# Performance work log

Measured on AMD Instinct MI355X. Metric: run time of the kernel, lower is better.

The kernel has to match this reference:

```python
import jax, jax.numpy as jnp
import numpy as np

S, B, D, H, FF, L, V, O = 512, 32, 512, 8, 2048, 6, 32000, 1000
DH = D // H
EPS = 1e-5


def layer_norm(x, g, b):
    mu = jnp.mean(x, axis=-1, keepdims=True)
    var = jnp.mean((x - mu) ** 2, axis=-1, keepdims=True)
    return (x - mu) * jax.lax.rsqrt(var + EPS) * g + b


def positional_encoding(seq_len, dim):
    pos = np.arange(seq_len, dtype=np.float32)[:, None]
    i = np.arange(dim)
    angle = pos / (10000.0 ** ((i // 2 * 2.0) / dim))
    pe = np.where(i % 2 == 0, np.sin(angle), np.cos(angle)).astype(np.float32)
    return jnp.asarray(pe)  # [seq_len, dim]


def setup_inputs() -> dict:
    key = jax.random.key(0)
    ks = jax.random.split(key, 16)
    sc = 0.02
    inp = {
        'x': jax.random.randint(ks[0], (S, B), 0, V, dtype=jnp.int32),
        'x_len': jnp.full((B,), S, dtype=jnp.int32),
        'emb': jax.random.normal(ks[1], (V, D), jnp.float32) * sc,
        'Wq': jax.random.normal(ks[2], (L, D, D), jnp.float32) * sc,
        'bq': jnp.zeros((L, D), jnp.float32),
        'Wk': jax.random.normal(ks[3], (L, D, D), jnp.float32) * sc,
        'bk': jnp.zeros((L, D), jnp.float32),
        'Wv': jax.random.normal(ks[4], (L, D, D), jnp.float32) * sc,
        'bv': jnp.zeros((L, D), jnp.float32),
        'Wo': jax.random.normal(ks[5], (L, D, D), jnp.float32) * sc,
        'bo': jnp.zeros((L, D), jnp.float32),
        'ln1_g': jnp.ones((L, D), jnp.float32),
        'ln1_b': jnp.zeros((L, D), jnp.float32),
        'W1': jax.random.normal(ks[6], (L, D, FF), jnp.float32) * sc,
        'b1': jnp.zeros((L, FF), jnp.float32),
        'W2': jax.random.normal(ks[7], (L, FF, D), jnp.float32) * sc,
        'b2': jnp.zeros((L, D), jnp.float32),
        'ln2_g': jnp.ones((L, D), jnp.float32),
        'ln2_b': jnp.zeros((L, D), jnp.float32),
        'W_fc': jax.random.normal(ks[8], (S * D, O), jnp.float32) * sc,
        'b_fc': jnp.zeros((O,), jnp.float32),
    }
    return inp


def reference(x, x_len, emb, Wq, bq, Wk, bk, Wv, bv, Wo, bo, ln1_g, ln1_b,
              W1, b1, W2, b2, ln2_g, ln2_b, W_fc, b_fc):
    out = emb[x]                      # [S, B, D]
    out = jnp.transpose(out, (1, 0, 2))  # [B, S, D]
    out = out + positional_encoding(S, D)[None, :, :]
    scale = DH ** -0.5
    for l in range(L):
        # NOTE: faithful to the original buggy head-split: plain row-major
        # reshape [B,S,D] -> [B*H,S,DH] without a [B,H,S,DH] transpose.
        q = jnp.reshape(out @ Wq[l] + bq[l], (B * H, S, DH))
        k = jnp.reshape(out @ Wk[l] + bk[l], (B * H, S, DH))
        v = jnp.reshape(out @ Wv[l] + bv[l], (B * H, S, DH))
        attn = jax.nn.softmax(jnp.einsum('gqd,gkd->gqk', q, k) * scale, axis=-1)
        ctx = jnp.einsum('gqk,gkd->gqd', attn, v).reshape(B, S, D)
        h = layer_norm(ctx @ Wo[l] + bo[l] + out, ln1_g[l], ln1_b[l])
        f = jax.nn.relu(h @ W1[l] + b1[l]) @ W2[l] + b2[l]
        out = layer_norm(f + h, ln2_g[l], ln2_b[l])
    out = out.reshape(B, S * D)
    return out @ W_fc + b_fc          # [B, O]
```

## Files before the change

### kernel.cpp

```cpp
#include <hip/hip_runtime.h>
#include <cstdint>
#include <cstddef>

#define S_  512
#define B_  32
#define D_  512
#define FF_ 2048
#define L_  6
#define O_  1000
#define M_  (B_*S_)
#define G_  256
#define DH_ 64

typedef __attribute__((ext_vector_type(8))) short bf16x8;
typedef __attribute__((ext_vector_type(4))) float f32x4;
typedef __attribute__((ext_vector_type(16))) float f32x16;

__device__ __forceinline__ unsigned short f2bf(float f) {
  unsigned int u = __builtin_bit_cast(unsigned int, f);
  u = (u + 0x7fffu + ((u >> 16) & 1u)) >> 16;
  return (unsigned short)u;
}
__device__ __forceinline__ float bf2f(unsigned short u) {
  return __builtin_bit_cast(float, (unsigned int)u << 16);
}
__device__ __forceinline__ unsigned int pkbf(float a, float b) {
  return (unsigned int)f2bf(a) | ((unsigned int)f2bf(b) << 16);
}
__device__ __forceinline__ unsigned int prm(float a, float b) {
  return __builtin_amdgcn_perm(__builtin_bit_cast(unsigned int, b),
                               __builtin_bit_cast(unsigned int, a), 0x07060302u);
}
__device__ __forceinline__ void gload_lds16(const void* g, void* l) {
  __builtin_amdgcn_global_load_lds(
      (const __attribute__((address_space(1))) unsigned int*)g,
      (__attribute__((address_space(3))) unsigned int*)l, 16, 0, 0);
}

__global__ void pe_kernel(float* __restrict__ pe) {
  int i = blockIdx.x * 256 + threadIdx.x;
  int s = i >> 9, d = i & 511;
  double de = (double)(d & ~1);
  double ang = (double)s * exp(de * (-9.210340371976184 / 512.0));
  pe[i] = (d & 1) ? (float)cos(ang) : (float)sin(ang);
}

__global__ void wconv_kernel(const float* __restrict__ W, unsigned short* __restrict__ Wt,
                             int K, int N, size_t ozs) {
  __shared__ float tile[32][33];
  const float* Wl = W + (size_t)blockIdx.z * K * N;
  unsigned short* Wtl = Wt + (size_t)blockIdx.z * ozs;
  int k0 = blockIdx.x * 32, n0 = blockIdx.y * 32;
  int c = threadIdx.x & 31, rb = threadIdx.x >> 5;
#pragma unroll
  for (int i = 0; i < 4; ++i) {
    int r = rb + i * 8;
    tile[r][c] = Wl[(size_t)(k0 + r) * N + n0 + c];
  }
  __syncthreads();
#pragma unroll
  for (int i = 0; i < 4; ++i) {
    int r = rb + i * 8;
    Wtl[(size_t)(n0 + r) * K + k0 + c] = f2bf(tile[c][r]);
  }
}

__global__ void embed_kernel(const int* __restrict__ x, const float* __restrict__ emb,
                             const float* __restrict__ pe, unsigned short* __restrict__ xb) {
  int bi = blockIdx.x;
  int s = bi / B_, b = bi % B_;
  int tok = x[s * B_ + b];
  int d = threadIdx.x * 4;
  float4 e = *(const float4*)(emb + (size_t)tok * D_ + d);
  float4 p = *(const float4*)(pe + (size_t)s * D_ + d);
  size_t o = ((size_t)b * S_ + s) * D_ + d;
  ushort4 u;
  u.x = f2bf(e.x + p.x); u.y = f2bf(e.y + p.y);
  u.z = f2bf(e.z + p.z); u.w = f2bf(e.w + p.w);
  *(ushort4*)(xb + o) = u;
}

__global__ __launch_bounds__(256, 2) void gemm_kernel(
    const unsigned short* __restrict__ A, const unsigned short* __restrict__ Bt,
    const float* __restrict__ b0, const float* __restrict__ b1, const float* __restrict__ b2,
    unsigned short* __restrict__ o0, unsigned short* __restrict__ o1, unsigned short* __restrict__ o2,
    int K, int N, int relu, int split, int nbx) {
  __shared__ unsigned short As[3][128 * 32];
  __shared__ unsigned short Bs[3][256 * 32];
  int nwg = nbx * (M_ / 128);
  int cpx = nwg >> 3;
  int id = blockIdx.x;
  int wg = (id & 7) * cpx + (id >> 3);
  int bx = wg % nbx, by = wg / nbx;
  int m0 = by * 128, n0 = bx * 256;

  int tid = threadIdx.x, lane = tid & 63, wid = tid >> 6;
  f32x4 acc[8][4];
#pragma unroll
  for (int mi = 0; mi < 8; ++mi)
#pragma unroll
    for (int ni = 0; ni < 4; ++ni) acc[mi][ni] = (f32x4)0.0f;

  int srow = lane >> 2, scol = (lane & 3) * 8;
  const unsigned short* Abase = A + (size_t)m0 * K;
  const unsigned short* Bbase = Bt + (size_t)n0 * K;
  int c16 = lane & 15, hi = lane >> 4;
  int koff = hi * 8;
  int brow = wid * 64 + c16;
  int nk = K >> 5;

  auto STAGE = [&](int kt, int bb) {
    int k0 = kt * 32;
#pragma unroll
    for (int i = 0; i < 6; ++i) {
      int c = wid * 6 + i;
      if (c < 8) {
        gload_lds16(Abase + (size_t)(c * 16 + srow) * K + k0 + scol, (char*)As[bb] + c * 1024);
      } else {
        int c2 = c - 8;
        gload_lds16(Bbase + (size_t)(c2 * 16 + srow) * K + k0 + scol, (char*)Bs[bb] + c2 * 1024);
      }
    }
  };

  STAGE(0, 0); STAGE(1, 1); STAGE(2, 2);
  int bb = 0;
  for (int kt = 0; kt < nk; ++kt) {
    int rem = nk - 1 - kt;
    if (rem >= 2)      asm volatile("s_waitcnt vmcnt(12)" ::: "memory");
    else if (rem == 1) asm volatile("s_waitcnt vmcnt(6)" ::: "memory");
    else               asm volatile("s_waitcnt vmcnt(0)" ::: "memory");
    __builtin_amdgcn_s_barrier();
    __builtin_amdgcn_sched_barrier(0);
    bf16x8 af[8], bfr[4];
#pragma unroll
    for (int mi = 0; mi < 8; ++mi) af[mi] = *(const bf16x8*)&As[bb][(mi * 16 + c16) * 32 + koff];
#pragma unroll
    for (int ni = 0; ni < 4; ++ni) bfr[ni] = *(const bf16x8*)&Bs[bb][(brow + ni * 16) * 32 + koff];
    __builtin_amdgcn_s_setprio(1);
#pragma unroll
    for (int mi = 0; mi < 8; ++mi)
#pragma unroll
      for (int ni = 0; ni < 4; ++ni)
        acc[mi][ni] = __builtin_amdgcn_mfma_f32_16x16x32_bf16(bfr[ni], af[mi], acc[mi][ni], 0, 0, 0);
    __builtin_amdgcn_s_setprio(0);
    __builtin_amdgcn_sched_barrier(0);
    __builtin_amdgcn_s_barrier();
    if (kt + 3 < nk) STAGE(kt + 3, bb);
    bb = (bb == 2) ? 0 : bb + 1;
  }

  const float* bias = b0;
  unsigned short* outb = o0;
  int nbase = n0, ostride = N;
  if (split) {
    int seg = n0 >> 9;
    if (seg == 1) { bias = b1; outb = o1; }
    else if (seg == 2) { bias = b2; outb = o2; }
    nbase = n0 & 511; ostride = 512;
  }
#pragma unroll
  for (int ni = 0; ni < 4; ++ni) {
    int colb = nbase + wid * 64 + ni * 16 + hi * 4;
    float4 bv = *(const float4*)(bias + colb);
#pragma unroll
    for (int mi = 0; mi < 8; ++mi) {
      int row = m0 + mi * 16 + c16;
      float v0 = acc[mi][ni][0] + bv.x;
      float v1 = acc[mi][ni][1] + bv.y;
      float v2 = acc[mi][ni][2] + bv.z;
      float v3 = acc[mi][ni][3] + bv.w;
      if (relu) { v0 = fmaxf(v0, 0.f); v1 = fmaxf(v1, 0.f); v2 = fmaxf(v2, 0.f); v3 = fmaxf(v3, 0.f); }
      *(uint2*)(outb + (size_t)row * ostride + colb) = make_uint2(pkbf(v0, v1), pkbf(v2, v3));
    }
  }
}

__global__ __launch_bounds__(128) void addln_kernel(
    const unsigned short* __restrict__ Y, const unsigned short* __restrict__ R,
    const float* __restrict__ g, const float* __restrict__ b,
    unsigned short* __restrict__ Out) {
  __shared__ float red[2], red2[2];
  int row = blockIdx.x, t = threadIdx.x;
  size_t o = (size_t)row * 512 + t * 4;
  ushort4 yv = *(const ushort4*)(Y + o);
  ushort4 rv = *(const ushort4*)(R + o);
  float v0 = bf2f(yv.x) + bf2f(rv.x);
  float v1 = bf2f(yv.y) + bf2f(rv.y);
  float v2 = bf2f(yv.z) + bf2f(rv.z);
  float v3 = bf2f(yv.w) + bf2f(rv.w);
  float s = v0 + v1 + v2 + v3;
#pragma unroll
  for (int m = 1; m < 64; m <<= 1) s += __shfl_xor(s, m);
  if ((t & 63) == 0) red[t >> 6] = s;
  __syncthreads();
  float mean = (red[0] + red[1]) * (1.0f / 512.0f);
  float d0 = v0 - mean, d1 = v1 - mean, d2 = v2 - mean, d3 = v3 - mean;
  float sq = d0 * d0 + d1 * d1 + d2 * d2 + d3 * d3;
#pragma unroll
  for (int m = 1; m < 64; m <<= 1) sq += __shfl_xor(sq, m);
  if ((t & 63) == 0) red2[t >> 6] = sq;
  __syncthreads();
  float var = (red2[0] + red2[1]) * (1.0f / 512.0f);
  float rstd = rsqrtf(var + 1e-5f);
  float4 gg = *(const float4*)(g + t * 4);
  float4 bb = *(const float4*)(b + t * 4);
  float y0 = d0 * rstd * gg.x + bb.x;
  float y1 = d1 * rstd * gg.y + bb.y;
  float y2 = d2 * rstd * gg.z + bb.z;
  float y3 = d3 * rstd * gg.w + bb.w;
  *(uint2*)(Out + o) = make_uint2(pkbf(y0, y1), pkbf(y2, y3));
}

__global__ __launch_bounds__(256) void attn_kernel(
    const unsigned short* __restrict__ Q, const unsigned short* __restrict__ Kb,
    const unsigned short* __restrict__ Vb, unsigned short* __restrict__ Ctx) {
  __shared__ char KlB[8192];
  __shared__ char VtB[8192];
  int g = blockIdx.y;
  int q0 = blockIdx.x * 256;
  const unsigned short* Kg = Kb + (size_t)g * 512 * 64;
  const unsigned short* Vg = Vb + (size_t)g * 512 * 64;
  int tid = threadIdx.x, lane = tid & 63, wid = tid >> 6;
  int l31 = lane & 31, h = lane >> 5;
  bool lo = (lane < 32);
  int qrowA = q0 + wid * 64 + l31;
  int qrowB = qrowA + 32;
  const float sc2 = 0.125f * 1.44269504f;

  bf16x8 qfa[4], qfb[4];
  {
    const unsigned short* qpa = Q + ((size_t)g * 512 + qrowA) * 64;
    const unsigned short* qpb = Q + ((size_t)g * 512 + qrowB) * 64;
#pragma unroll
    for (int c = 0; c < 4; ++c) {
      bf16x8 ra = *(const bf16x8*)(qpa + c * 16 + h * 8);
      bf16x8 rb = *(const bf16x8*)(qpb + c * 16 + h * 8);
      union { unsigned int u[4]; bf16x8 v; } ua, ub;
#pragma unroll
      for (int j = 0; j < 4; ++j) {
        ua.u[j] = pkbf(bf2f((unsigned short)ra[2 * j]) * sc2,
                       bf2f((unsigned short)ra[2 * j + 1]) * sc2);
        ub.u[j] = pkbf(bf2f((unsigned short)rb[2 * j]) * sc2,
                       bf2f((unsigned short)rb[2 * j + 1]) * sc2);
      }
      qfa[c] = ua.v; qfb[c] = ub.v;
    }
  }

  f32x16 cA0 = (f32x16)0.0f, cA1 = (f32x16)0.0f;
  f32x16 cB0 = (f32x16)0.0f, cB1 = (f32x16)0.0f;
  float mrA = -3.0e38f, lsA = 0.0f;
  float mrB = -3.0e38f, lsB = 0.0f;

  for (int kt = 0; kt < 8; ++kt) {
    __syncthreads();
    {
      int row = tid >> 2;
      size_t base = (size_t)(kt * 64 + row) * 64;
#pragma unroll
      for (int i = 0; i < 2; ++i) {
        int cb = ((tid & 3) + 4 * i) * 16;
        bf16x8 kv = *(const bf16x8*)(Kg + base + cb / 2);
        *(bf16x8*)(KlB + row * 128 + (cb ^ ((row & 7) << 4))) = kv;
        bf16x8 vv = *(const bf16x8*)(Vg + base + cb / 2);
#pragma unroll
        for (int j = 0; j < 8; ++j) {
          int d = cb / 2 + j;
          *(unsigned short*)(VtB + d * 128 + ((2 * row) ^ ((d & 7) << 4))) =
              (unsigned short)vv[j];
        }
      }
    }
    __syncthreads();

#pragma unroll
    for (int sub = 0; sub < 2; ++sub) {
      f32x16 s0 = (f32x16)0.0f, s1 = (f32x16)0.0f;
#pragma unroll
      for (int c = 0; c < 4; ++c) {
        int cb = 32 * c + 16 * h;
        int sw = cb ^ ((l31 & 7) << 4);
        bf16x8 k0 = *(const bf16x8*)(KlB + l31 * 128 + sw);
        bf16x8 k1 = *(const bf16x8*)(KlB + (32 + l31) * 128 + sw);
        bf16x8 qf = sub ? qfb[c] : qfa[c];
        s0 = __builtin_amdgcn_mfma_f32_32x32x16_bf16(k0, qf, s0, 0, 0, 0);
        s1 = __builtin_amdgcn_mfma_f32_32x32x16_bf16(k1, qf, s1, 0, 0, 0);
      }

      float mr = sub ? mrB : mrA;
      float ls = sub ? lsB : lsA;
      float pm = s0[0];
#pragma unroll
      for (int i = 1; i < 16; ++i) pm = fmaxf(pm, s0[i]);
#pragma unroll
      for (int i = 0; i < 16; ++i) pm = fmaxf(pm, s1[i]);
      pm = fmaxf(pm, __shfl_xor(pm, 32));
      if (!__all(pm <= mr + 8.0f)) {
        float mnew = fmaxf(mr, pm);
        float alpha = exp2f(mr - mnew);
        ls *= alpha;
        if (sub) {
#pragma unroll
          for (int i = 0; i < 16; ++i) { cB0[i] *= alpha; cB1[i] *= alpha; }
        } else {
#pragma unroll
          for (int i = 0; i < 16; ++i) { cA0[i] *= alpha; cA1[i] *= alpha; }
        }
        mr = mnew;
      }
      float p[32];
      float rs = 0.0f;
#pragma unroll
      for (int i = 0; i < 16; ++i) { p[i] = exp2f(s0[i] - mr); rs += p[i]; }
#pragma unroll
      for (int i = 0; i < 16; ++i) { p[16 + i] = exp2f(s1[i] - mr); rs += p[16 + i]; }
      float rso = __shfl_xor(rs, 32);
      ls += rs + rso;
      if (sub) { mrB = mr; lsB = ls; } else { mrA = mr; lsA = ls; }

      union { unsigned int u[4]; bf16x8 v; } pa[4];
#pragma unroll
      for (int t = 0; t < 2; ++t) {
#pragma unroll
        for (int u = 0; u < 2; ++u) {
#pragma unroll
          for (int pr = 0; pr < 2; ++pr) {
            const int b0i = t * 16 + 8 * u;
            unsigned int a  = prm(p[b0i + 2 * pr],     p[b0i + 2 * pr + 1]);
            unsigned int b  = prm(p[b0i + 4 + 2 * pr], p[b0i + 4 + 2 * pr + 1]);
            unsigned int sa = __shfl_xor(a, 32);
            unsigned int sb = __shfl_xor(b, 32);
            pa[t * 2 + u].u[pr]     = lo ? a  : sb;
            pa[t * 2 + u].u[2 + pr] = lo ? sa : b;
          }
        }
      }

#pragma unroll
      for (int kc = 0; kc < 4; ++kc) {
        int cb = 32 * kc + 16 * h;
        int sw = cb ^ ((l31 & 7) << 4);
        bf16x8 v0 = *(const bf16x8*)(VtB + l31 * 128 + sw);
        bf16x8 v1 = *(const bf16x8*)(VtB + (32 + l31) * 128 + sw);
        if (sub) {
          cB0 = __builtin_amdgcn_mfma_f32_32x32x16_bf16(v0, pa[kc].v, cB0, 0, 0, 0);
          cB1 = __builtin_amdgcn_mfma_f32_32x32x16_bf16(v1, pa[kc].v, cB1, 0, 0, 0);
        } else {
          cA0 = __builtin_amdgcn_mfma_f32_32x32x16_bf16(v0, pa[kc].v, cA0, 0, 0, 0);
          cA1 = __builtin_amdgcn_mfma_f32_32x32x16_bf16(v1, pa[kc].v, cA1, 0, 0, 0);
        }
      }
    }
  }

#pragma unroll
  for (int sub = 0; sub < 2; ++sub) {
    float inv = 1.0f / (sub ? lsB : lsA);
    int qrow = sub ? qrowB : qrowA;
    unsigned short* cp = Ctx + ((size_t)g * 512 + qrow) * 64;
#pragma unroll
    for (int dh = 0; dh < 2; ++dh) {
#pragma unroll
      for (int rq = 0; rq < 4; ++rq) {
        float e0 = (sub ? (dh ? cB1[rq * 4 + 0] : cB0[rq * 4 + 0]) : (dh ? cA1[rq * 4 + 0] : cA0[rq * 4 + 0])) * inv;
        float e1 = (sub ? (dh ? cB1[rq * 4 + 1] : cB0[rq * 4 + 1]) : (dh ? cA1[rq * 4 + 1] : cA0[rq * 4 + 1])) * inv;
        float e2 = (sub ? (dh ? cB1[rq * 4 + 2] : cB0[rq * 4 + 2]) : (dh ? cA1[rq * 4 + 2] : cA0[rq * 4 + 2])) * inv;
        float e3 = (sub ? (dh ? cB1[rq * 4 + 3] : cB0[rq * 4 + 3]) : (dh ? cA1[rq * 4 + 3] : cA0[rq * 4 + 3])) * inv;
        int d0 = dh * 32 + rq * 8 + h * 4;
        *(uint2*)(cp + d0) = make_uint2(pkbf(e0, e1), pkbf(e2, e3));
      }
    }
  }
}

#define KCH 1024
__global__ __launch_bounds__(512) void fc_part_kernel(const unsigned short* __restrict__ act,
                                                      const float* __restrict__ Wfc,
                                                      float* __restrict__ part) {
  __shared__ float al[32][256];
  int t = threadIdx.x;
  int kc = blockIdx.x;
  size_t k0 = (size_t)kc * KCH;
  int o1 = t;
  int o2 = 512 + t;
  bool a2 = (o2 < O_);
  float acc1[32], acc2[32];
#pragma unroll
  for (int bb = 0; bb < 32; ++bb) { acc1[bb] = 0.0f; acc2[bb] = 0.0f; }
  for (int sub = 0; sub < KCH / 256; ++sub) {
    __syncthreads();
    for (int i = t; i < 32 * 128; i += 512) {
      int bb = i >> 7, kk = (i & 127) * 2;
      ushort2 u = *(const ushort2*)(act + (size_t)bb * 262144 + k0 + sub * 256 + kk);
      al[bb][kk] = bf2f(u.x);
      al[bb][kk + 1] = bf2f(u.y);
    }
    __syncthreads();
    const float* wp = Wfc + (k0 + sub * 256) * O_;
    for (int kk = 0; kk < 256; kk += 4) {
      const float* wr = wp + (size_t)kk * O_;
      float w10 = wr[o1];
      float w11 = wr[O_ + o1];
      float w12 = wr[2 * O_ + o1];
      float w13 = wr[3 * O_ + o1];
      float w20 = a2 ? wr[o2] : 0.0f;
      float w21 = a2 ? wr[O_ + o2] : 0.0f;
      float w22 = a2 ? wr[2 * O_ + o2] : 0.0f;
      float w23 = a2 ? wr[3 * O_ + o2] : 0.0f;
#pragma unroll
      for (int bb = 0; bb < 32; ++bb) {
        f32x4 av = *(const f32x4*)&al[bb][kk];
        acc1[bb] = fmaf(av[0], w10, acc1[bb]);
        acc1[bb] = fmaf(av[1], w11, acc1[bb]);
        acc1[bb] = fmaf(av[2], w12, acc1[bb]);
        acc1[bb] = fmaf(av[3], w13, acc1[bb]);
        acc2[bb] = fmaf(av[0], w20, acc2[bb]);
        acc2[bb] = fmaf(av[1], w21, acc2[bb]);
        acc2[bb] = fmaf(av[2], w22, acc2[bb]);
        acc2[bb] = fmaf(av[3], w23, acc2[bb]);
      }
    }
  }
#pragma unroll
  for (int bb = 0; bb < 32; ++bb) {
    part[((size_t)kc * 32 + bb) * O_ + o1] = acc1[bb];
    if (a2) part[((size_t)kc * 32 + bb) * O_ + o2] = acc2[bb];
  }
}

__global__ void fc_reduce_kernel(const float* __restrict__ part, const float* __restrict__ bfc,
                                 float* __restrict__ out) {
  int o = blockIdx.x * 256 + threadIdx.x;
  int b = blockIdx.y;
  if (o >= O_) return;
  float s = bfc[o];
  for (int c = 0; c < 256; ++c) s += part[((size_t)c * 32 + b) * O_ + o];
  out[(size_t)b * O_ + o] = s;
}

extern "C" void kernel_launch(void* const* d_in, const int* in_sizes, int n_in,
                              void* d_out, int out_size, void* d_ws, size_t ws_size,
                              hipStream_t stream) {
  const int*   x   = (const int*)d_in[0];
  const float* emb = (const float*)d_in[2];
  const float* Wq  = (const float*)d_in[3];
  const float* bq  = (const float*)d_in[4];
  const float* Wk  = (const float*)d_in[5];
  const float* bk  = (const float*)d_in[6];
  const float* Wv  = (const float*)d_in[7];
  const float* bv  = (const float*)d_in[8];
  const float* Wo  = (const float*)d_in[9];
  const float* bo  = (const float*)d_in[10];
  const float* g1  = (const float*)d_in[11];
  const float* bn1 = (const float*)d_in[12];
  const float* W1  = (const float*)d_in[13];
  const float* bf1 = (const float*)d_in[14];
  const float* W2  = (const float*)d_in[15];
  const float* bf2 = (const float*)d_in[16];
  const float* g2  = (const float*)d_in[17];
  const float* bn2 = (const float*)d_in[18];
  const float* Wfc = (const float*)d_in[19];
  const float* bfc = (const float*)d_in[20];
  float* out = (float*)d_out;

  char* ws = (char*)d_ws;
  size_t off = 0;
  auto take = [&](size_t bytes) { char* p = ws + off; off += (bytes + 255) & ~(size_t)255; return p; };
  float*          pe   = (float*)take((size_t)512 * 512 * 4);
  unsigned short* wqkv = (unsigned short*)take((size_t)L_ * 1536 * 512 * 2);
  unsigned short* wot  = (unsigned short*)take((size_t)L_ * 512 * 512 * 2);
  unsigned short* w1t  = (unsigned short*)take((size_t)L_ * 2048 * 512 * 2);
  unsigned short* w2t  = (unsigned short*)take((size_t)L_ * 512 * 2048 * 2);
  unsigned short* xb   = (unsigned short*)take((size_t)M_ * 512 * 2);
  unsigned short* qb   = (unsigned short*)take((size_t)M_ * 512 * 2);
  unsigned short* kb   = (unsigned short*)take((size_t)M_ * 512 * 2);
  unsigned short* vb   = (unsigned short*)take((size_t)M_ * 512 * 2);
  unsigned short* cxb  = (unsigned short*)take((size_t)M_ * 512 * 2);
  unsigned short* hb   = (unsigned short*)take((size_t)M_ * 512 * 2);
  unsigned short* t1   = (unsigned short*)take((size_t)M_ * 512 * 2);
  unsigned short* f1b  = qb;
  float*          part = (float*)qb;

  pe_kernel<<<1024, 256, 0, stream>>>(pe);
  wconv_kernel<<<dim3(16, 16, L_), 256, 0, stream>>>(Wq, wqkv,          512, 512,  (size_t)1536 * 512);
  wconv_kernel<<<dim3(16, 16, L_), 256, 0, stream>>>(Wk, wqkv + 262144, 512, 512,  (size_t)1536 * 512);
  wconv_kernel<<<dim3(16, 16, L_), 256, 0, stream>>>(Wv, wqkv + 524288, 512, 512,  (size_t)1536 * 512);
  wconv_kernel<<<dim3(16, 16, L_), 256, 0, stream>>>(Wo, wot,           512, 512,  (size_t)512 * 512);
  wconv_kernel<<<dim3(16, 64, L_), 256, 0, stream>>>(W1, w1t,           512, 2048, (size_t)2048 * 512);
  wconv_kernel<<<dim3(64, 16, L_), 256, 0, stream>>>(W2, w2t,           2048, 512, (size_t)512 * 2048);
  embed_kernel<<<M_, 128, 0, stream>>>(x, emb, pe, xb);

  for (int l = 0; l < L_; ++l) {
    gemm_kernel<<<768, 256, 0, stream>>>(
        xb, wqkv + (size_t)l * 1536 * 512,
        bq + l * 512, bk + l * 512, bv + l * 512,
        qb, kb, vb, 512, 1536, 0, 1, 6);
    attn_kernel<<<dim3(2, G_), 256, 0, stream>>>(qb, kb, vb, cxb);
    gemm_kernel<<<256, 256, 0, stream>>>(
        cxb, wot + (size_t)l * 512 * 512,
        bo + l * 512, nullptr, nullptr,
        t1, nullptr, nullptr, 512, 512, 0, 0, 2);
    addln_kernel<<<M_, 128, 0, stream>>>(t1, xb, g1 + l * 512, bn1 + l * 512, hb);
    gemm_kernel<<<1024, 256, 0, stream>>>(
        hb, w1t + (size_t)l * 2048 * 512,
        bf1 + l * 2048, nullptr, nullptr,
        f1b, nullptr, nullptr, 512, 2048, 1, 0, 8);
    gemm_kernel<<<256, 256, 0, stream>>>(
        f1b, w2t + (size_t)l * 512 * 2048,
        bf2 + l * 512, nullptr, nullptr,
        t1, nullptr, nullptr, 2048, 512, 0, 0, 2);
    addln_kernel<<<M_, 128, 0, stream>>>(t1, hb, g2 + l * 512, bn2 + l * 512, xb);
  }

  fc_part_kernel<<<256, 512, 0, stream>>>(xb, Wfc, part);
  fc_reduce_kernel<<<dim3(4, 32), 256, 0, stream>>>(part, bfc, out);
}
```

Baseline: 1.942 ms.

## Split-K the N=512 GEMMs into fp32 partials reduced inside add+LayerNorm

The Wo and W2 projection GEMMs (N=512) launched only 256 workgroups, which underfills the MI355X's 256 CUs at two blocks per CU. They now use split-K with two K halves, giving 512 workgroups that write fp32 partial tiles. A new add+LayerNorm kernel sums both partials, the bias and the residual before normalizing. This trades extra fp32 traffic (writing and reading 2×M×512 floats) for better CU occupancy, and it also drops one bf16 rounding step.

```diff
diff --git a/kernel.cpp b/kernel.cpp
--- a/kernel.cpp
+++ b/kernel.cpp
@@ -84,15 +84,18 @@
     const unsigned short* __restrict__ A, const unsigned short* __restrict__ Bt,
     const float* __restrict__ b0, const float* __restrict__ b1, const float* __restrict__ b2,
     unsigned short* __restrict__ o0, unsigned short* __restrict__ o1, unsigned short* __restrict__ o2,
-    int K, int N, int relu, int split, int nbx) {
+    float* __restrict__ pout,
+    int K, int N, int relu, int split, int nbx, int kspl) {
   __shared__ unsigned short As[3][128 * 32];
   __shared__ unsigned short Bs[3][256 * 32];
-  int nwg = nbx * (M_ / 128);
+  int nwg = nbx * (M_ / 128) * kspl;
   int cpx = nwg >> 3;
   int id = blockIdx.x;
   int wg = (id & 7) * cpx + (id >> 3);
+  int kq = wg % kspl; wg /= kspl;
   int bx = wg % nbx, by = wg / nbx;
   int m0 = by * 128, n0 = bx * 256;
+  int Ks = K / kspl;
 
   int tid = threadIdx.x, lane = tid & 63, wid = tid >> 6;
   f32x4 acc[8][4];
@@ -102,12 +105,12 @@
     for (int ni = 0; ni < 4; ++ni) acc[mi][ni] = (f32x4)0.0f;
 
   int srow = lane >> 2, scol = (lane & 3) * 8;
-  const unsigned short* Abase = A + (size_t)m0 * K;
-  const unsigned short* Bbase = Bt + (size_t)n0 * K;
+  const unsigned short* Abase = A + (size_t)m0 * K + kq * Ks;
+  const unsigned short* Bbase = Bt + (size_t)n0 * K + kq * Ks;
   int c16 = lane & 15, hi = lane >> 4;
   int koff = hi * 8;
   int brow = wid * 64 + c16;
-  int nk = K >> 5;
+  int nk = Ks >> 5;
 
   auto STAGE = [&](int kt, int bb) {
     int k0 = kt * 32;
@@ -150,6 +153,19 @@
     bb = (bb == 2) ? 0 : bb + 1;
   }
 
+  if (pout) {
+#pragma unroll
+    for (int ni = 0; ni < 4; ++ni) {
+      int colb = n0 + wid * 64 + ni * 16 + hi * 4;
+#pragma unroll
+      for (int mi = 0; mi < 8; ++mi) {
+        int row = m0 + mi * 16 + c16;
+        *(f32x4*)(pout + ((size_t)kq * M_ + row) * N + colb) = acc[mi][ni];
+      }
+    }
+    return;
+  }
+
   const float* bias = b0;
   unsigned short* outb = o0;
   int nbase = n0, ostride = N;
@@ -176,19 +192,22 @@
   }
 }
 
-__global__ __launch_bounds__(128) void addln_kernel(
-    const unsigned short* __restrict__ Y, const unsigned short* __restrict__ R,
-    const float* __restrict__ g, const float* __restrict__ b,
+__global__ __launch_bounds__(128) void addln2_kernel(
+    const float* __restrict__ P, const unsigned short* __restrict__ R,
+    const float* __restrict__ bias,
+    const float* __restrict__ gamma, const float* __restrict__ beta,
     unsigned short* __restrict__ Out) {
   __shared__ float red[2], red2[2];
   int row = blockIdx.x, t = threadIdx.x;
   size_t o = (size_t)row * 512 + t * 4;
-  ushort4 yv = *(const ushort4*)(Y + o);
+  float4 p0 = *(const float4*)(P + o);
+  float4 p1 = *(const float4*)(P + (size_t)M_ * 512 + o);
+  float4 bv = *(const float4*)(bias + t * 4);
   ushort4 rv = *(const ushort4*)(R + o);
-  float v0 = bf2f(yv.x) + bf2f(rv.x);
-  float v1 = bf2f(yv.y) + bf2f(rv.y);
-  float v2 = bf2f(yv.z) + bf2f(rv.z);
-  float v3 = bf2f(yv.w) + bf2f(rv.w);
+  float v0 = p0.x + p1.x + bv.x + bf2f(rv.x);
+  float v1 = p0.y + p1.y + bv.y + bf2f(rv.y);
+  float v2 = p0.z + p1.z + bv.z + bf2f(rv.z);
+  float v3 = p0.w + p1.w + bv.w + bf2f(rv.w);
   float s = v0 + v1 + v2 + v3;
 #pragma unroll
   for (int m = 1; m < 64; m <<= 1) s += __shfl_xor(s, m);
@@ -203,8 +222,8 @@
   __syncthreads();
   float var = (red2[0] + red2[1]) * (1.0f / 512.0f);
   float rstd = rsqrtf(var + 1e-5f);
-  float4 gg = *(const float4*)(g + t * 4);
-  float4 bb = *(const float4*)(b + t * 4);
+  float4 gg = *(const float4*)(gamma + t * 4);
+  float4 bb = *(const float4*)(beta + t * 4);
   float y0 = d0 * rstd * gg.x + bb.x;
   float y1 = d1 * rstd * gg.y + bb.y;
   float y2 = d2 * rstd * gg.z + bb.z;
@@ -478,7 +497,7 @@
   unsigned short* vb   = (unsigned short*)take((size_t)M_ * 512 * 2);
   unsigned short* cxb  = (unsigned short*)take((size_t)M_ * 512 * 2);
   unsigned short* hb   = (unsigned short*)take((size_t)M_ * 512 * 2);
-  unsigned short* t1   = (unsigned short*)take((size_t)M_ * 512 * 2);
+  float*          pf   = (float*)take((size_t)2 * M_ * 512 * 4);
   unsigned short* f1b  = qb;
   float*          part = (float*)qb;
 
@@ -495,22 +514,22 @@
     gemm_kernel<<<768, 256, 0, stream>>>(
         xb, wqkv + (size_t)l * 1536 * 512,
         bq + l * 512, bk + l * 512, bv + l * 512,
-        qb, kb, vb, 512, 1536, 0, 1, 6);
+        qb, kb, vb, nullptr, 512, 1536, 0, 1, 6, 1);
     attn_kernel<<<dim3(2, G_), 256, 0, stream>>>(qb, kb, vb, cxb);
-    gemm_kernel<<<256, 256, 0, stream>>>(
+    gemm_kernel<<<512, 256, 0, stream>>>(
         cxb, wot + (size_t)l * 512 * 512,
-        bo + l * 512, nullptr, nullptr,
-        t1, nullptr, nullptr, 512, 512, 0, 0, 2);
-    addln_kernel<<<M_, 128, 0, stream>>>(t1, xb, g1 + l * 512, bn1 + l * 512, hb);
+        nullptr, nullptr, nullptr,
+        nullptr, nullptr, nullptr, pf, 512, 512, 0, 0, 2, 2);
+    addln2_kernel<<<M_, 128, 0, stream>>>(pf, xb, bo + l * 512, g1 + l * 512, bn1 + l * 512, hb);
     gemm_kernel<<<1024, 256, 0, stream>>>(
         hb, w1t + (size_t)l * 2048 * 512,
         bf1 + l * 2048, nullptr, nullptr,
-        f1b, nullptr, nullptr, 512, 2048, 1, 0, 8);
-    gemm_kernel<<<256, 256, 0, stream>>>(
+        f1b, nullptr, nullptr, nullptr, 512, 2048, 1, 0, 8, 1);
+    gemm_kernel<<<512, 256, 0, stream>>>(
         f1b, w2t + (size_t)l * 512 * 2048,
-        bf2 + l * 512, nullptr, nullptr,
-        t1, nullptr, nullptr, 2048, 512, 0, 0, 2);
-    addln_kernel<<<M_, 128, 0, stream>>>(t1, hb, g2 + l * 512, bn2 + l * 512, xb);
+        nullptr, nullptr, nullptr,
+        nullptr, nullptr, nullptr, pf, 2048, 512, 0, 0, 2, 2);
+    addln2_kernel<<<M_, 128, 0, stream>>>(pf, hb, bf2 + l * 512, g2 + l * 512, bn2 + l * 512, xb);
   }
 
   fc_part_kernel<<<256, 512, 0, stream>>>(xb, Wfc, part);
```

New measurement: 2.008 ms. +3.4%, slower.

## Add 128x128-tile GEMM kernel for N=512 projections to fill more CUs

Applied to the files above, without the earlier changes.

Adds a new GEMM kernel with 128x128 output tiles, a 3-stage LDS pipeline and a 2x2 wave layout. It is used for the output projection and the FFN down-projection, where N=512. The old kernel launched only 256 workgroups for these, which is roughly one wave of work on the 256 CUs. Smaller tiles give 512 workgroups with 2 blocks per CU, aiming at better occupancy and load balance. The cost is less operand reuse per tile, so global and LDS traffic per FLOP goes up.

```diff
diff --git a/kernel.cpp b/kernel.cpp
--- a/kernel.cpp
+++ b/kernel.cpp
@@ -172,6 +172,88 @@
       float v3 = acc[mi][ni][3] + bv.w;
       if (relu) { v0 = fmaxf(v0, 0.f); v1 = fmaxf(v1, 0.f); v2 = fmaxf(v2, 0.f); v3 = fmaxf(v3, 0.f); }
       *(uint2*)(outb + (size_t)row * ostride + colb) = make_uint2(pkbf(v0, v1), pkbf(v2, v3));
+    }
+  }
+}
+
+__global__ __launch_bounds__(256, 2) void gemm128_kernel(
+    const unsigned short* __restrict__ A, const unsigned short* __restrict__ Bt,
+    const float* __restrict__ bias, unsigned short* __restrict__ outb,
+    int K, int N, int nbx) {
+  __shared__ unsigned short As[3][128 * 32];
+  __shared__ unsigned short Bs[3][128 * 32];
+  int nwg = nbx * (M_ / 128);
+  int cpx = nwg >> 3;
+  int id = blockIdx.x;
+  int wg = (id & 7) * cpx + (id >> 3);
+  int bx = wg % nbx, by = wg / nbx;
+  int m0 = by * 128, n0 = bx * 128;
+
+  int tid = threadIdx.x, lane = tid & 63, wid = tid >> 6;
+  int wm = wid >> 1, wn = wid & 1;
+  f32x4 acc[4][4];
+#pragma unroll
+  for (int mi = 0; mi < 4; ++mi)
+#pragma unroll
+    for (int ni = 0; ni < 4; ++ni) acc[mi][ni] = (f32x4)0.0f;
+
+  int srow = lane >> 2, scol = (lane & 3) * 8;
+  const unsigned short* Abase = A + (size_t)m0 * K;
+  const unsigned short* Bbase = Bt + (size_t)n0 * K;
+  int c16 = lane & 15, hi = lane >> 4;
+  int koff = hi * 8;
+  int arow = wm * 64 + c16, brow = wn * 64 + c16;
+  int nk = K >> 5;
+
+  auto STAGE = [&](int kt, int bb) {
+    int k0 = kt * 32;
+#pragma unroll
+    for (int i = 0; i < 2; ++i) {
+      int c = wid * 2 + i;
+      gload_lds16(Abase + (size_t)(c * 16 + srow) * K + k0 + scol, (char*)As[bb] + c * 1024);
+      gload_lds16(Bbase + (size_t)(c * 16 + srow) * K + k0 + scol, (char*)Bs[bb] + c * 1024);
+    }
+  };
+
+  STAGE(0, 0); STAGE(1, 1); STAGE(2, 2);
+  int bb = 0;
+  for (int kt = 0; kt < nk; ++kt) {
+    int rem = nk - 1 - kt;
+    if (rem >= 2)      asm volatile("s_waitcnt vmcnt(8)" ::: "memory");
+    else if (rem == 1) asm volatile("s_waitcnt vmcnt(4)" ::: "memory");
+    else               asm volatile("s_waitcnt vmcnt(0)" ::: "memory");
+    __builtin_amdgcn_s_barrier();
+    __builtin_amdgcn_sched_barrier(0);
+    bf16x8 af[4], bfr[4];
+#pragma unroll
+    for (int mi = 0; mi < 4; ++mi) af[mi] = *(const bf16x8*)&As[bb][(arow + mi * 16) * 32 + koff];
+#pragma unroll
+    for (int ni = 0; ni < 4; ++ni) bfr[ni] = *(const bf16x8*)&Bs[bb][(brow + ni * 16) * 32 + koff];
+    __builtin_amdgcn_s_setprio(1);
+#pragma unroll
+    for (int mi = 0; mi < 4; ++mi)
+#pragma unroll
+      for (int ni = 0; ni < 4; ++ni)
+        acc[mi][ni] = __builtin_amdgcn_mfma_f32_16x16x32_bf16(bfr[ni], af[mi], acc[mi][ni], 0, 0, 0);
+    __builtin_amdgcn_s_setprio(0);
+    __builtin_amdgcn_sched_barrier(0);
+    __builtin_amdgcn_s_barrier();
+    if (kt + 3 < nk) STAGE(kt + 3, bb);
+    bb = (bb == 2) ? 0 : bb + 1;
+  }
+
+#pragma unroll
+  for (int ni = 0; ni < 4; ++ni) {
+    int colb = n0 + wn * 64 + ni * 16 + hi * 4;
+    float4 bv = *(const float4*)(bias + colb);
+#pragma unroll
+    for (int mi = 0; mi < 4; ++mi) {
+      int row = m0 + wm * 64 + mi * 16 + c16;
+      float v0 = acc[mi][ni][0] + bv.x;
+      float v1 = acc[mi][ni][1] + bv.y;
+      float v2 = acc[mi][ni][2] + bv.z;
+      float v3 = acc[mi][ni][3] + bv.w;
+      *(uint2*)(outb + (size_t)row * N + colb) = make_uint2(pkbf(v0, v1), pkbf(v2, v3));
     }
   }
 }
@@ -497,19 +579,15 @@
         bq + l * 512, bk + l * 512, bv + l * 512,
         qb, kb, vb, 512, 1536, 0, 1, 6);
     attn_kernel<<<dim3(2, G_), 256, 0, stream>>>(qb, kb, vb, cxb);
-    gemm_kernel<<<256, 256, 0, stream>>>(
-        cxb, wot + (size_t)l * 512 * 512,
-        bo + l * 512, nullptr, nullptr,
-        t1, nullptr, nullptr, 512, 512, 0, 0, 2);
+    gemm128_kernel<<<512, 256, 0, stream>>>(
+        cxb, wot + (size_t)l * 512 * 512, bo + l * 512, t1, 512, 512, 4);
     addln_kernel<<<M_, 128, 0, stream>>>(t1, xb, g1 + l * 512, bn1 + l * 512, hb);
     gemm_kernel<<<1024, 256, 0, stream>>>(
         hb, w1t + (size_t)l * 2048 * 512,
         bf1 + l * 2048, nullptr, nullptr,
         f1b, nullptr, nullptr, 512, 2048, 1, 0, 8);
-    gemm_kernel<<<256, 256, 0, stream>>>(
-        f1b, w2t + (size_t)l * 512 * 2048,
-        bf2 + l * 512, nullptr, nullptr,
-        t1, nullptr, nullptr, 2048, 512, 0, 0, 2);
+    gemm128_kernel<<<512, 256, 0, stream>>>(
+        f1b, w2t + (size_t)l * 512 * 2048, bf2 + l * 512, t1, 2048, 512, 4);
     addln_kernel<<<M_, 128, 0, stream>>>(t1, hb, g2 + l * 512, bn2 + l * 512, xb);
   }
 
```

Measured after the change: 1.915 ms. About the same (-1.4%).
